# Kernel optimization log

Hardware: AMD Instinct MI355X
Metric: run time of the kernel (lower is better)

## Reference

```python
import jax, jax.numpy as jnp
import numpy as np

B, T, C = 2, 192, 512
H, D = 8, 64  # num_heads, head_dim; inner_dim = H*D = C


def setup_inputs() -> dict:
    key = jax.random.key(0)
    k1, k2, k3 = jax.random.split(key, 3)
    x = jax.random.normal(k1, (B, T, C), dtype=jnp.float32)
    W_in = jax.random.normal(k2, (C, 5 * H * D), dtype=jnp.float32) * 0.02
    b_in = jnp.zeros((5 * H * D,), dtype=jnp.float32)
    W_out = jax.random.normal(k3, (H * D, C), dtype=jnp.float32) * 0.02
    b_out = jnp.zeros((C,), dtype=jnp.float32)
    return {"x": x, "W_in": W_in, "b_in": b_in, "W_out": W_out, "b_out": b_out}


def _split_heads(t):
    # (B,T,H*D) -> (B,H,T,D)
    return t.reshape(B, T, H, D).transpose(0, 2, 1, 3)


def reference(x, W_in, b_in, W_out, b_out):
    scale = D ** -0.5
    proj = x @ W_in + b_in  # (B,T,5*H*D)
    q, k1, v1, k2, v2 = jnp.split(proj, 5, axis=-1)
    q = _split_heads(q) * scale
    k1 = _split_heads(k1)
    v1 = _split_heads(v1)
    k2 = _split_heads(k2)
    v2 = _split_heads(v2)
    # trilinear logits: <q_i, k1_j, k2_k> / sqrt(D), computed in fp32
    logits = jnp.einsum('bhid,bhjd,bhkd->bhijk', q, k1, k2,
                        preferred_element_type=jnp.float32)
    # softmax over the joint (j,k) axes
    attn = jax.nn.softmax(logits.reshape(B, H, T, T * T), axis=-1)
    attn = attn.reshape(B, H, T, T, T).astype(x.dtype)
    # out_i[d] = sum_{j,k} attn[i,j,k] * v1_j[d] * v2_k[d]
    out = jnp.einsum('bhijk,bhjd,bhkd->bhid', attn, v1, v2)
    y = out.transpose(0, 2, 1, 3).reshape(B, T, H * D)  # merge heads
    return y @ W_out + b_out
```

## Files before the change

kernel.cpp:

```cpp
#include <hip/hip_runtime.h>
#include <hip/hip_bf16.h>


typedef float  v4f __attribute__((ext_vector_type(4)));
typedef short  v8s __attribute__((ext_vector_type(8)));

__device__ __forceinline__ unsigned short f2bf(float f) {
  unsigned u = __float_as_uint(f);
  u += 0x7fffu + ((u >> 16) & 1u);
  return (unsigned short)(u >> 16);
}
__device__ __forceinline__ float bf2f(unsigned short b) {
  return __uint_as_float(((unsigned)b) << 16);
}
__device__ __forceinline__ unsigned pack_bf16(float lo, float hi) {
  __hip_bfloat162 t = __float22bfloat162_rn(float2{lo, hi});
  union { __hip_bfloat162 b; unsigned u; } cv;
  cv.b = t;
  return cv.u;
}

#if __has_builtin(__builtin_amdgcn_exp2f)
#define EXP2F(x) __builtin_amdgcn_exp2f(x)
#else
#define EXP2F(x) exp2f(x)
#endif

#define MFMA32(a, b, c) __builtin_amdgcn_mfma_f32_16x16x32_bf16((a), (b), (c), 0, 0, 0)

#define QSCALE 0.18033688011112042f


#define XH_OFF   589824
#define XL_OFF   786432
#define WTH_OFF  983040
#define WTL_OFF  2293760
#define WOTH_OFF 3604480
#define WOTL_OFF 3866624
#define OH_OFF   4128768
#define OL_OFF   4325376

__device__ __forceinline__ int v1perm(int t) {
  return (t & ~31) | (((t >> 2) & 3) << 3) | ((t & 3) << 1) | ((t >> 4) & 1);
}

__global__ __launch_bounds__(256) void prep_kernel(
    const float* __restrict__ x, const float* __restrict__ Win,
    const float* __restrict__ Wout, unsigned short* __restrict__ wsh) {
  __shared__ float tile[32 * 65];
  const int bi = blockIdx.x, t = threadIdx.x;
  if (bi < 768) {
    const float* W; unsigned short *Th, *Tl; int R, n0, k0;
    if (bi < 640) {
      W = Win; Th = wsh + WTH_OFF; Tl = wsh + WTL_OFF; R = 2560;
      n0 = (bi % 40) << 6; k0 = (bi / 40) << 5;
    } else {
      const int idx = bi - 640;
      W = Wout; Th = wsh + WOTH_OFF; Tl = wsh + WOTL_OFF; R = 512;
      n0 = (idx & 7) << 6; k0 = (idx >> 3) << 5;
    }
    const int n = t & 63, kq = (t >> 6) * 8;
#pragma unroll
    for (int j = 0; j < 8; ++j)
      tile[(kq + j) * 65 + n] = W[(k0 + kq + j) * R + n0 + n];
    __syncthreads();
    const int n2 = t >> 2, ks = (t & 3) * 8;
    union { uint4 u; unsigned short us[8]; } ph, pl;
#pragma unroll
    for (int j = 0; j < 8; ++j) {
      const float v = tile[(ks + j) * 65 + n2];
      const unsigned short h = f2bf(v);
      ph.us[j] = h;
      pl.us[j] = f2bf(v - bf2f(h));
    }
    *(uint4*)(Th + (n0 + n2) * 512 + k0 + ks) = ph.u;
    *(uint4*)(Tl + (n0 + n2) * 512 + k0 + ks) = pl.u;
  } else {
    const int flat = ((bi - 768) * 256 + t) * 8;
    const v4f v0 = *(const v4f*)(x + flat);
    const v4f v1 = *(const v4f*)(x + flat + 4);
    union { uint4 u; unsigned short us[8]; } ph, pl;
#pragma unroll
    for (int j = 0; j < 4; ++j) {
      unsigned short h = f2bf(v0[j]);
      ph.us[j] = h; pl.us[j] = f2bf(v0[j] - bf2f(h));
      h = f2bf(v1[j]);
      ph.us[4 + j] = h; pl.us[4 + j] = f2bf(v1[j] - bf2f(h));
    }
    *(uint4*)(wsh + XH_OFF + flat) = ph.u;
    *(uint4*)(wsh + XL_OFF + flat) = pl.u;
  }
}

__global__ __launch_bounds__(64) void proj_kernel(
    const unsigned short* __restrict__ wsh, const float* __restrict__ bin,
    float* __restrict__ wsf, unsigned short* __restrict__ wshd) {
  const int lane = threadIdx.x;
  const int c = lane & 15, q = lane >> 4;
  const int bm = blockIdx.x % 12, bn = blockIdx.x / 12;

  const unsigned short* base[8];
  base[0] = wsh + XH_OFF + (bm * 32 + c) * 512 + (q << 3);
  base[1] = base[0] + 16 * 512;
  base[2] = wsh + XL_OFF + (bm * 32 + c) * 512 + (q << 3);
  base[3] = base[2] + 16 * 512;
  base[4] = wsh + WTH_OFF + (bn * 32 + c) * 512 + (q << 3);
  base[5] = base[4] + 16 * 512;
  base[6] = wsh + WTL_OFF + (bn * 32 + c) * 512 + (q << 3);
  base[7] = base[6] + 16 * 512;

  const v4f z = {0.f, 0.f, 0.f, 0.f};
  v4f a00 = z, a01 = z, a10 = z, a11 = z;

  v8s cur[8], nxt[8];
#pragma unroll
  for (int i = 0; i < 8; ++i) cur[i] = *(const v8s*)(base[i]);
#pragma unroll
  for (int i = 0; i < 8; ++i) nxt[i] = *(const v8s*)(base[i] + 32);

#pragma unroll 1
  for (int ks = 0; ks < 16; ++ks) {
    v8s nx2[8];
    if (ks < 14) {
      const int o = (ks + 2) * 32;
#pragma unroll
      for (int i = 0; i < 8; ++i) nx2[i] = *(const v8s*)(base[i] + o);
    }
    a00 = MFMA32(cur[2], cur[4], a00); a00 = MFMA32(cur[0], cur[6], a00); a00 = MFMA32(cur[0], cur[4], a00);
    a01 = MFMA32(cur[2], cur[5], a01); a01 = MFMA32(cur[0], cur[7], a01); a01 = MFMA32(cur[0], cur[5], a01);
    a10 = MFMA32(cur[3], cur[4], a10); a10 = MFMA32(cur[1], cur[6], a10); a10 = MFMA32(cur[1], cur[4], a10);
    a11 = MFMA32(cur[3], cur[5], a11); a11 = MFMA32(cur[1], cur[7], a11); a11 = MFMA32(cur[1], cur[5], a11);
#pragma unroll
    for (int i = 0; i < 8; ++i) { cur[i] = nxt[i]; nxt[i] = nx2[i]; }
  }

  v4f accs[2][2] = {{a00, a01}, {a10, a11}};
#pragma unroll
  for (int mt = 0; mt < 2; ++mt) {
#pragma unroll
    for (int nt = 0; nt < 2; ++nt) {
      const int n = bn * 32 + nt * 16 + c;
      const int which = n >> 9, cc = n & 511, h = cc >> 6, d = cc & 63;
      const float bv = bin[n];
#pragma unroll
      for (int r = 0; r < 4; ++r) {
        const int m = bm * 32 + mt * 16 + (q << 2) + r;
        const int b = (m >= 192) ? 1 : 0;
        const int tt = m - (b ? 192 : 0);
        const int bh = b * 8 + h;
        const float val = accs[mt][nt][r] + bv;
        const int rm = ((bh * 192 + tt) << 6) + d;
        if (which == 0)      wsf[rm] = val * QSCALE;
        else if (which == 1) wshd[rm] = f2bf(val);
        else if (which == 2) wshd[393216 + ((bh << 6) + d) * 192 + v1perm(tt)] = f2bf(val);
        else if (which == 3) wshd[196608 + rm] = f2bf(val);
        else wsf[196608 + ((bh * 192 + tt) * 16 + (d & 15)) * 4 + (d >> 4)] = val;
      }
    }
  }
}

__global__ __launch_bounds__(256, 2) void attn_kernel(
    const float* __restrict__ wsf, const unsigned short* __restrict__ wsh,
    float* __restrict__ accp, float* __restrict__ Sp) {
  __shared__ char smem[52224];
  unsigned short* V1s = (unsigned short*)smem;

  const int tid  = threadIdx.x;
  const int wv   = tid >> 6;
  const int lane = tid & 63;
  const int c    = lane & 15;
  const int quad = lane >> 4;

  const int bb = blockIdx.x;
  const int kb = bb & 3;
  const int it = (bb >> 2) % 12;
  const int bh = bb / 48;

  const unsigned short* k1g = wsh + bh * 192 * 64;
  const unsigned short* v1g = wsh + 393216 + bh * 64 * 192;
  const unsigned short* k2g = wsh + 196608 + bh * 192 * 64;
  const float*          v2g = wsf + 196608 + bh * 12288;

  for (int idx = tid; idx < 1536; idx += 256) {
    const int r = idx / 24, c8 = (idx % 24) * 8;
    *(uint4*)(V1s + r * 200 + c8) = *(const uint4*)(v1g + r * 192 + c8);
  }

  v8s k1f[12][2];
#pragma unroll
  for (int jt = 0; jt < 12; ++jt) {
    const unsigned short* kp = k1g + ((jt * 16 + c) << 6) + (quad << 3);
    k1f[jt][0] = *(const v8s*)(kp);
    k1f[jt][1] = *(const v8s*)(kp + 32);
  }

  const float* qg = wsf + ((bh * 192 + it * 16 + c) << 6) + (quad << 3);
  float q0[8], q1[8];
  {
    v4f qa = *(const v4f*)(qg), qb = *(const v4f*)(qg + 4);
    v4f qc = *(const v4f*)(qg + 32), qd = *(const v4f*)(qg + 36);
#pragma unroll
    for (int e = 0; e < 4; ++e) {
      q0[e] = qa[e]; q0[4 + e] = qb[e];
      q1[e] = qc[e]; q1[4 + e] = qd[e];
    }
  }
  __syncthreads();

  unsigned* Pw = (unsigned*)(smem + 25600) + wv * 1664;
  const v4f z = {0.f, 0.f, 0.f, 0.f};
  v4f acc[4] = {z, z, z, z};
  v4f oSA = z, oSB = z;
  const short one = (short)0x3F80;
  const v8s ones = {one, one, one, one, one, one, one, one};

  const int kloc0 = wv * 12;
  const unsigned short* k2r = k2g + ((kb * 48 + kloc0) << 6) + (quad << 3);
  union U4 { uint4 u4; unsigned short us[8]; };
  union AF { v8s v; unsigned u[4]; };

#pragma unroll 1
  for (int p = 0; p < 6; ++p) {
    const int rA = kloc0 + 2 * p, rB = rA + 1;
    U4 klA, khA, klB, khB;
    klA.u4 = *(const uint4*)(k2r + p * 128);
    khA.u4 = *(const uint4*)(k2r + p * 128 + 32);
    klB.u4 = *(const uint4*)(k2r + p * 128 + 64);
    khB.u4 = *(const uint4*)(k2r + p * 128 + 96);
    const v4f v2A = *(const v4f*)(v2g + (((kb * 48 + rA) << 4) + c) * 4);
    const v4f v2B = *(const v4f*)(v2g + (((kb * 48 + rB) << 4) + c) * 4);

    AF af[2][2];
#pragma unroll
    for (int e = 0; e < 4; ++e) {
      af[0][0].u[e] = pack_bf16(q0[2*e] * bf2f(klA.us[2*e]), q0[2*e+1] * bf2f(klA.us[2*e+1]));
      af[0][1].u[e] = pack_bf16(q1[2*e] * bf2f(khA.us[2*e]), q1[2*e+1] * bf2f(khA.us[2*e+1]));
      af[1][0].u[e] = pack_bf16(q0[2*e] * bf2f(klB.us[2*e]), q0[2*e+1] * bf2f(klB.us[2*e+1]));
      af[1][1].u[e] = pack_bf16(q1[2*e] * bf2f(khB.us[2*e]), q1[2*e+1] * bf2f(khB.us[2*e+1]));
    }

    v4f oA[4] = {z, z, z, z}, oB[4] = {z, z, z, z};

#pragma unroll
    for (int h = 0; h < 2; ++h) {
#pragma unroll
      for (int kk = 0; kk < 2; ++kk) {
        v4f C[6];
#pragma unroll
        for (int jj = 0; jj < 6; ++jj) {
          const int jt = h * 6 + jj;
          v4f t0 = MFMA32(af[kk][0].v, k1f[jt][0], z);
          C[jj] = MFMA32(af[kk][1].v, k1f[jt][1], t0);
        }
#pragma unroll
        for (int jj = 0; jj < 6; ++jj)
#pragma unroll
          for (int r = 0; r < 4; ++r) C[jj][r] = EXP2F(C[jj][r]);
#pragma unroll
        for (int m = 0; m < 3; ++m)
#pragma unroll
          for (int r = 0; r < 4; ++r)
            Pw[kk * 832 + ((quad << 2) + r) * 52 + m * 16 + c] =
                pack_bf16(C[2*m][r], C[2*m+1][r]);
      }
#pragma unroll
      for (int m = 0; m < 3; ++m) {
        const v8s apA = *(const v8s*)(Pw + c * 52 + m * 16 + (quad << 2));
        const v8s apB = *(const v8s*)(Pw + 832 + c * 52 + m * 16 + (quad << 2));
        oSA = MFMA32(apA, ones, oSA);
        oSB = MFMA32(apB, ones, oSB);
        const int vcol = (h * 3 + m) * 32 + (quad << 3);
#pragma unroll
        for (int t = 0; t < 4; ++t) {
          const v8s vf = *(const v8s*)(V1s + (c + 16 * t) * 200 + vcol);
          oA[t] = MFMA32(apA, vf, oA[t]);
          oB[t] = MFMA32(apB, vf, oB[t]);
        }
      }
    }
#pragma unroll
    for (int t = 0; t < 4; ++t) acc[t] += oA[t] * v2A[t] + oB[t] * v2B[t];
  }

  __syncthreads();
  float* redA = (float*)smem;
  float* redS = (float*)smem + 4096;

  if (c == 0) {
    float* rs = redS + wv * 16 + (quad << 2);
#pragma unroll
    for (int r = 0; r < 4; ++r) rs[r] = oSA[r] + oSB[r];
  }
#pragma unroll
  for (int r = 0; r < 4; ++r) {
    float* rr = redA + wv * 1024 + (((quad << 2) + r) << 6) + c;
    rr[0] = acc[0][r]; rr[16] = acc[1][r]; rr[32] = acc[2][r]; rr[48] = acc[3][r];
  }
  __syncthreads();

  const int pbase = (bh * 12 + it) * 4 + kb;
  float* ap_out = accp + pbase * 1024;
  for (int idx = tid; idx < 1024; idx += 256)
    ap_out[idx] = redA[idx] + redA[1024 + idx] + redA[2048 + idx] + redA[3072 + idx];
  if (tid < 16)
    Sp[pbase * 16 + tid] = redS[tid] + redS[16 + tid] + redS[32 + tid] + redS[48 + tid];
}

__global__ __launch_bounds__(256) void norm_kernel(
    const float* __restrict__ accp, const float* __restrict__ Sp,
    unsigned short* __restrict__ wsh) {
  const int flat = blockIdx.x * 2048 + threadIdx.x * 8;
  const int m = flat >> 9, cc = flat & 511;
  const int b = (m >= 192) ? 1 : 0;
  const int tt = m - (b ? 192 : 0);
  const int h = cc >> 6, d0 = cc & 63;
  const int bh = b * 8 + h, it = tt >> 4, i = tt & 15;
  const int pb = (bh * 12 + it) * 4;
  const float* ap = accp + pb * 1024 + (i << 6) + d0;
  v4f a0 = *(const v4f*)(ap), a1 = *(const v4f*)(ap + 4);
  float Sv = Sp[pb * 16 + i];
#pragma unroll
  for (int kb = 1; kb < 4; ++kb) {
    a0 += *(const v4f*)(ap + kb * 1024);
    a1 += *(const v4f*)(ap + kb * 1024 + 4);
    Sv += Sp[(pb + kb) * 16 + i];
  }
  const float inv = 1.0f / Sv;
  union { uint4 u; unsigned short us[8]; } ph, pl;
#pragma unroll
  for (int j = 0; j < 4; ++j) {
    float v = a0[j] * inv;
    unsigned short hh = f2bf(v);
    ph.us[j] = hh; pl.us[j] = f2bf(v - bf2f(hh));
    v = a1[j] * inv;
    hh = f2bf(v);
    ph.us[4 + j] = hh; pl.us[4 + j] = f2bf(v - bf2f(hh));
  }
  *(uint4*)(wsh + OH_OFF + flat) = ph.u;
  *(uint4*)(wsh + OL_OFF + flat) = pl.u;
}

__global__ __launch_bounds__(64) void outp_kernel(
    const unsigned short* __restrict__ wsh, const float* __restrict__ bout,
    float* __restrict__ y) {
  const int lane = threadIdx.x;
  const int c = lane & 15, q = lane >> 4;
  const int bm = blockIdx.x % 12, bn = blockIdx.x / 12;

  const unsigned short* base[8];
  base[0] = wsh + OH_OFF + (bm * 32 + c) * 512 + (q << 3);
  base[1] = base[0] + 16 * 512;
  base[2] = wsh + OL_OFF + (bm * 32 + c) * 512 + (q << 3);
  base[3] = base[2] + 16 * 512;
  base[4] = wsh + WOTH_OFF + (bn * 32 + c) * 512 + (q << 3);
  base[5] = base[4] + 16 * 512;
  base[6] = wsh + WOTL_OFF + (bn * 32 + c) * 512 + (q << 3);
  base[7] = base[6] + 16 * 512;

  const v4f z = {0.f, 0.f, 0.f, 0.f};
  v4f a00 = z, a01 = z, a10 = z, a11 = z;

  v8s cur[8], nxt[8];
#pragma unroll
  for (int i = 0; i < 8; ++i) cur[i] = *(const v8s*)(base[i]);
#pragma unroll
  for (int i = 0; i < 8; ++i) nxt[i] = *(const v8s*)(base[i] + 32);

#pragma unroll 1
  for (int ks = 0; ks < 16; ++ks) {
    v8s nx2[8];
    if (ks < 14) {
      const int o = (ks + 2) * 32;
#pragma unroll
      for (int i = 0; i < 8; ++i) nx2[i] = *(const v8s*)(base[i] + o);
    }
    a00 = MFMA32(cur[2], cur[4], a00); a00 = MFMA32(cur[0], cur[6], a00); a00 = MFMA32(cur[0], cur[4], a00);
    a01 = MFMA32(cur[2], cur[5], a01); a01 = MFMA32(cur[0], cur[7], a01); a01 = MFMA32(cur[0], cur[5], a01);
    a10 = MFMA32(cur[3], cur[4], a10); a10 = MFMA32(cur[1], cur[6], a10); a10 = MFMA32(cur[1], cur[4], a10);
    a11 = MFMA32(cur[3], cur[5], a11); a11 = MFMA32(cur[1], cur[7], a11); a11 = MFMA32(cur[1], cur[5], a11);
#pragma unroll
    for (int i = 0; i < 8; ++i) { cur[i] = nxt[i]; nxt[i] = nx2[i]; }
  }

  v4f accs[2][2] = {{a00, a01}, {a10, a11}};
#pragma unroll
  for (int mt = 0; mt < 2; ++mt) {
#pragma unroll
    for (int nt = 0; nt < 2; ++nt) {
      const int n = bn * 32 + nt * 16 + c;
      const float bv = bout[n];
#pragma unroll
      for (int r = 0; r < 4; ++r) {
        const int m = bm * 32 + mt * 16 + (q << 2) + r;
        y[m * 512 + n] = accs[mt][nt][r] + bv;
      }
    }
  }
}

extern "C" void kernel_launch(void* const* d_in, const int* in_sizes, int n_in,
                              void* d_out, int out_size, void* d_ws, size_t ws_size,
                              hipStream_t stream) {
  const float* x    = (const float*)d_in[0];
  const float* Win  = (const float*)d_in[1];
  const float* bin  = (const float*)d_in[2];
  const float* Wout = (const float*)d_in[3];
  const float* bout = (const float*)d_in[4];

  float* wsf = (float*)d_ws;
  unsigned short* wsh = (unsigned short*)(wsf + 1191936);
  float* accp = wsf + 393216;
  float* Sp   = wsf + 1179648;

  prep_kernel<<<dim3(864), 256, 0, stream>>>(x, Win, Wout, wsh);
  proj_kernel<<<dim3(960), 64, 0, stream>>>(wsh, bin, wsf, wsh);
  attn_kernel<<<dim3(768), 256, 0, stream>>>(wsf, wsh, accp, Sp);
  norm_kernel<<<dim3(96), 256, 0, stream>>>(accp, Sp, wsh);
  outp_kernel<<<dim3(192), 64, 0, stream>>>(wsh, bout, (float*)d_out);
}
```

Measured before the change: 150.1 us.

## Split attn waves over j and k halves, keep V1 fragments in registers

Each wave now owns half of the j tiles (jh) and half of the block's k rows (kh), instead of all j tiles for 12 k rows. This lets each wave hold only 6 K1 tiles plus its V1 fragments in registers, so V1 no longer needs LDS staging and its per-iteration LDS reads go away. K2 rows are staged once in LDS instead. Shared memory shrinks substantially. The trade-off is a 24-step loop that processes one k row per iteration, with a short serial chain (MFMA, exp, P store to LDS, reload, MFMA) per j pair. That gives less instruction-level parallelism than the previous two-row batches and may expose latency.

Measured after the change: 150.4 us. About the same (+0.2%).

```diff
diff --git a/kernel.cpp b/kernel.cpp
--- a/kernel.cpp
+++ b/kernel.cpp
@@ -163,14 +163,16 @@
 __global__ __launch_bounds__(256, 2) void attn_kernel(
     const float* __restrict__ wsf, const unsigned short* __restrict__ wsh,
     float* __restrict__ accp, float* __restrict__ Sp) {
-  __shared__ char smem[52224];
-  unsigned short* V1s = (unsigned short*)smem;
+  __shared__ char smem[16640];
+  unsigned short* K2s = (unsigned short*)smem;
 
   const int tid  = threadIdx.x;
   const int wv   = tid >> 6;
   const int lane = tid & 63;
   const int c    = lane & 15;
   const int quad = lane >> 4;
+  const int jh   = wv & 1;
+  const int kh   = wv >> 1;
 
   const int bb = blockIdx.x;
   const int kb = bb & 3;
@@ -182,18 +184,25 @@
   const unsigned short* k2g = wsh + 196608 + bh * 192 * 64;
   const float*          v2g = wsf + 196608 + bh * 12288;
 
-  for (int idx = tid; idx < 1536; idx += 256) {
-    const int r = idx / 24, c8 = (idx % 24) * 8;
-    *(uint4*)(V1s + r * 200 + c8) = *(const uint4*)(v1g + r * 192 + c8);
-  }
-
-  v8s k1f[12][2];
-#pragma unroll
-  for (int jt = 0; jt < 12; ++jt) {
-    const unsigned short* kp = k1g + ((jt * 16 + c) << 6) + (quad << 3);
-    k1f[jt][0] = *(const v8s*)(kp);
-    k1f[jt][1] = *(const v8s*)(kp + 32);
-  }
+  for (int idx = tid; idx < 384; idx += 256) {
+    const int r = idx >> 3, c8 = (idx & 7) * 8;
+    *(uint4*)(K2s + r * 64 + c8) = *(const uint4*)(k2g + (kb * 48 + r) * 64 + c8);
+  }
+
+  v8s k1f[6][2];
+#pragma unroll
+  for (int j = 0; j < 6; ++j) {
+    const unsigned short* kp = k1g + (((jh * 6 + j) * 16 + c) << 6) + (quad << 3);
+    k1f[j][0] = *(const v8s*)(kp);
+    k1f[j][1] = *(const v8s*)(kp + 32);
+  }
+
+  v8s vf[3][4];
+#pragma unroll
+  for (int m = 0; m < 3; ++m)
+#pragma unroll
+    for (int t = 0; t < 4; ++t)
+      vf[m][t] = *(const v8s*)(v1g + (c + 16 * t) * 192 + ((jh * 3 + m) << 5) + (quad << 3));
 
   const float* qg = wsf + ((bh * 192 + it * 16 + c) << 6) + (quad << 3);
   float q0[8], q1[8];
@@ -208,79 +217,54 @@
   }
   __syncthreads();
 
-  unsigned* Pw = (unsigned*)(smem + 25600) + wv * 1664;
+  unsigned* Pw = (unsigned*)(smem + 6144) + wv * 320;
   const v4f z = {0.f, 0.f, 0.f, 0.f};
   v4f acc[4] = {z, z, z, z};
-  v4f oSA = z, oSB = z;
+  v4f oS = z;
   const short one = (short)0x3F80;
   const v8s ones = {one, one, one, one, one, one, one, one};
 
-  const int kloc0 = wv * 12;
-  const unsigned short* k2r = k2g + ((kb * 48 + kloc0) << 6) + (quad << 3);
   union U4 { uint4 u4; unsigned short us[8]; };
   union AF { v8s v; unsigned u[4]; };
 
 #pragma unroll 1
-  for (int p = 0; p < 6; ++p) {
-    const int rA = kloc0 + 2 * p, rB = rA + 1;
-    U4 klA, khA, klB, khB;
-    klA.u4 = *(const uint4*)(k2r + p * 128);
-    khA.u4 = *(const uint4*)(k2r + p * 128 + 32);
-    klB.u4 = *(const uint4*)(k2r + p * 128 + 64);
-    khB.u4 = *(const uint4*)(k2r + p * 128 + 96);
-    const v4f v2A = *(const v4f*)(v2g + (((kb * 48 + rA) << 4) + c) * 4);
-    const v4f v2B = *(const v4f*)(v2g + (((kb * 48 + rB) << 4) + c) * 4);
-
-    AF af[2][2];
+  for (int ks = 0; ks < 24; ++ks) {
+    const int rl = kh * 24 + ks;
+    U4 kl, khh;
+    kl.u4  = *(const uint4*)(K2s + (rl << 6) + (quad << 3));
+    khh.u4 = *(const uint4*)(K2s + (rl << 6) + (quad << 3) + 32);
+    const v4f v2v = *(const v4f*)(v2g + (((kb * 48 + rl) << 4) + c) * 4);
+
+    AF af0, af1;
 #pragma unroll
     for (int e = 0; e < 4; ++e) {
-      af[0][0].u[e] = pack_bf16(q0[2*e] * bf2f(klA.us[2*e]), q0[2*e+1] * bf2f(klA.us[2*e+1]));
-      af[0][1].u[e] = pack_bf16(q1[2*e] * bf2f(khA.us[2*e]), q1[2*e+1] * bf2f(khA.us[2*e+1]));
-      af[1][0].u[e] = pack_bf16(q0[2*e] * bf2f(klB.us[2*e]), q0[2*e+1] * bf2f(klB.us[2*e+1]));
-      af[1][1].u[e] = pack_bf16(q1[2*e] * bf2f(khB.us[2*e]), q1[2*e+1] * bf2f(khB.us[2*e+1]));
-    }
-
-    v4f oA[4] = {z, z, z, z}, oB[4] = {z, z, z, z};
-
-#pragma unroll
-    for (int h = 0; h < 2; ++h) {
-#pragma unroll
-      for (int kk = 0; kk < 2; ++kk) {
-        v4f C[6];
-#pragma unroll
-        for (int jj = 0; jj < 6; ++jj) {
-          const int jt = h * 6 + jj;
-          v4f t0 = MFMA32(af[kk][0].v, k1f[jt][0], z);
-          C[jj] = MFMA32(af[kk][1].v, k1f[jt][1], t0);
-        }
-#pragma unroll
-        for (int jj = 0; jj < 6; ++jj)
-#pragma unroll
-          for (int r = 0; r < 4; ++r) C[jj][r] = EXP2F(C[jj][r]);
-#pragma unroll
-        for (int m = 0; m < 3; ++m)
-#pragma unroll
-          for (int r = 0; r < 4; ++r)
-            Pw[kk * 832 + ((quad << 2) + r) * 52 + m * 16 + c] =
-                pack_bf16(C[2*m][r], C[2*m+1][r]);
-      }
-#pragma unroll
-      for (int m = 0; m < 3; ++m) {
-        const v8s apA = *(const v8s*)(Pw + c * 52 + m * 16 + (quad << 2));
-        const v8s apB = *(const v8s*)(Pw + 832 + c * 52 + m * 16 + (quad << 2));
-        oSA = MFMA32(apA, ones, oSA);
-        oSB = MFMA32(apB, ones, oSB);
-        const int vcol = (h * 3 + m) * 32 + (quad << 3);
-#pragma unroll
-        for (int t = 0; t < 4; ++t) {
-          const v8s vf = *(const v8s*)(V1s + (c + 16 * t) * 200 + vcol);
-          oA[t] = MFMA32(apA, vf, oA[t]);
-          oB[t] = MFMA32(apB, vf, oB[t]);
-        }
-      }
-    }
-#pragma unroll
-    for (int t = 0; t < 4; ++t) acc[t] += oA[t] * v2A[t] + oB[t] * v2B[t];
+      af0.u[e] = pack_bf16(q0[2*e] * bf2f(kl.us[2*e]),  q0[2*e+1] * bf2f(kl.us[2*e+1]));
+      af1.u[e] = pack_bf16(q1[2*e] * bf2f(khh.us[2*e]), q1[2*e+1] * bf2f(khh.us[2*e+1]));
+    }
+
+    v4f o0 = z, o1 = z, o2 = z, o3 = z;
+#pragma unroll
+    for (int m = 0; m < 3; ++m) {
+      v4f Ca = MFMA32(af0.v, k1f[2*m][0], z);
+      Ca = MFMA32(af1.v, k1f[2*m][1], Ca);
+      v4f Cb = MFMA32(af0.v, k1f[2*m+1][0], z);
+      Cb = MFMA32(af1.v, k1f[2*m+1][1], Cb);
+#pragma unroll
+      for (int r = 0; r < 4; ++r) { Ca[r] = EXP2F(Ca[r]); Cb[r] = EXP2F(Cb[r]); }
+#pragma unroll
+      for (int r = 0; r < 4; ++r)
+        Pw[((quad << 2) + r) * 20 + c] = pack_bf16(Ca[r], Cb[r]);
+      const v8s ap = *(const v8s*)(Pw + c * 20 + (quad << 2));
+      oS = MFMA32(ap, ones, oS);
+      o0 = MFMA32(ap, vf[m][0], o0);
+      o1 = MFMA32(ap, vf[m][1], o1);
+      o2 = MFMA32(ap, vf[m][2], o2);
+      o3 = MFMA32(ap, vf[m][3], o3);
+    }
+    acc[0] += o0 * v2v[0];
+    acc[1] += o1 * v2v[1];
+    acc[2] += o2 * v2v[2];
+    acc[3] += o3 * v2v[3];
   }
 
   __syncthreads();
@@ -290,7 +274,7 @@
   if (c == 0) {
     float* rs = redS + wv * 16 + (quad << 2);
 #pragma unroll
-    for (int r = 0; r < 4; ++r) rs[r] = oSA[r] + oSB[r];
+    for (int r = 0; r < 4; ++r) rs[r] = oS[r];
   }
 #pragma unroll
   for (int r = 0; r < 4; ++r) {
```
